# Performance work log

Hardware: AMD Instinct MI355X
Metric: run time of the kernel (lower is better)

## Reference

```python
import jax, jax.numpy as jnp
import numpy as np

HEADS = 4
HEAD_DIM = 32  # out_features // heads = 128 // 4


def setup_inputs() -> dict:
    key = jax.random.key(0)
    k1, k2, k3, k4 = jax.random.split(key, 4)
    N, IN_F = 200000, 128
    E = 500  # <= 1000 so no edge subsampling; loop covers min(E,500)=all edges
    x = jax.random.normal(k1, (N, IN_F), dtype=jnp.float32)
    edge_index = jax.random.randint(k2, (2, E), 0, N, dtype=jnp.int64)
    # Linear weight [out=heads*head_dim, in] as in torch nn.Linear
    W = jax.random.normal(k3, (HEADS * HEAD_DIM, IN_F), dtype=jnp.float32) * (1.0 / np.sqrt(IN_F))
    a = jax.random.normal(k4, (HEADS, 2 * HEAD_DIM), dtype=jnp.float32) * 0.1
    return {"x": x, "edge_index": edge_index, "W": W, "a": a}


def reference(x, edge_index, W, a):
    N = x.shape[0]
    h = (x @ W.T).reshape(N, HEADS, HEAD_DIM)  # [N, H, D]
    src, dst = edge_index[0], edge_index[1]
    h_src = h[src]  # [E, H, D]
    h_dst = h[dst]  # [E, H, D]
    edge_h = jnp.concatenate([h_src, h_dst], axis=-1)  # [E, H, 2D]
    attn = jnp.sum(edge_h * a, axis=-1)  # [E, H]
    attn = jax.nn.leaky_relu(attn, negative_slope=0.2)
    # out[dst] += 0.1 * attn * h[src], accumulated over duplicate dst
    out = h.at[dst].add(0.1 * attn[:, :, None] * h_src)
    return out.reshape(N, HEADS * HEAD_DIM)  # dropout is identity in eval
```

## Files before the change

kernel.cpp:

```cpp
#include <hip/hip_runtime.h>
#include <hip/hip_bf16.h>


typedef __attribute__((ext_vector_type(8))) short bf16x8;
typedef __attribute__((ext_vector_type(4))) float f32x4;

#define W_PAD 136

__global__ __launch_bounds__(256, 3) void gat_gemm_kernel(
    const float* __restrict__ x,
    const float* __restrict__ W,
    float* __restrict__ out,
    int N) {
  __shared__ __hip_bfloat16 Ws[128 * W_PAD];
  __shared__ __hip_bfloat16 Xs[64 * W_PAD];

  const int tid = threadIdx.x;

  #pragma unroll
  for (int it = 0; it < 16; ++it) {
    int seg = tid + it * 256;
    int row = seg >> 5;
    int off = (seg & 31) * 4;
    float4 v = *reinterpret_cast<const float4*>(&W[row * 128 + off]);
    union { ushort4 u4; __hip_bfloat16 h[4]; } wpk;
    wpk.h[0] = __float2bfloat16(v.x);
    wpk.h[1] = __float2bfloat16(v.y);
    wpk.h[2] = __float2bfloat16(v.z);
    wpk.h[3] = __float2bfloat16(v.w);
    *reinterpret_cast<ushort4*>(&Ws[row * W_PAD + off]) = wpk.u4;
  }
  __syncthreads();

  const int wave = tid >> 6;
  const int lane = tid & 63;
  const int m = lane & 15;
  const int q = lane >> 4;

  const int T64 = N >> 6;
  const int stride = (int)gridDim.x;
  int t = (int)blockIdx.x;

  float4 rA[8];
  {
    const float* xt = x + (long)t * 8192;
    #pragma unroll
    for (int i = 0; i < 8; ++i)
      rA[i] = *reinterpret_cast<const float4*>(xt + (i * 256 + tid) * 4);
  }

  while (true) {
    #pragma unroll
    for (int i = 0; i < 8; ++i) {
      int g = i * 256 + tid;
      union { ushort4 u4; __hip_bfloat16 h[4]; } p;
      p.h[0] = __float2bfloat16(rA[i].x);
      p.h[1] = __float2bfloat16(rA[i].y);
      p.h[2] = __float2bfloat16(rA[i].z);
      p.h[3] = __float2bfloat16(rA[i].w);
      *reinterpret_cast<ushort4*>(&Xs[(g >> 5) * W_PAD + (g & 31) * 4]) = p.u4;
    }

    const int tn = t + stride;
    if (tn < T64) {
      const float* xn = x + (long)tn * 8192;
      #pragma unroll
      for (int i = 0; i < 8; ++i)
        rA[i] = *reinterpret_cast<const float4*>(xn + (i * 256 + tid) * 4);
    }

    asm volatile("s_waitcnt lgkmcnt(0)" ::: "memory");
    __builtin_amdgcn_sched_barrier(0);
    __builtin_amdgcn_s_barrier();

    bf16x8 af[4];
    #pragma unroll
    for (int s = 0; s < 4; ++s)
      af[s] = *reinterpret_cast<const bf16x8*>(
          &Xs[(wave * 16 + m) * W_PAD + s * 32 + q * 8]);

    f32x4 acc[8];
    #pragma unroll
    for (int nt = 0; nt < 8; ++nt) acc[nt] = (f32x4){0.f, 0.f, 0.f, 0.f};
    #pragma unroll
    for (int s = 0; s < 4; ++s) {
      #pragma unroll
      for (int nt = 0; nt < 8; ++nt) {
        bf16x8 wfrag = *reinterpret_cast<const bf16x8*>(
            &Ws[(nt * 16 + m) * W_PAD + s * 32 + q * 8]);
        acc[nt] = __builtin_amdgcn_mfma_f32_16x16x32_bf16(wfrag, af[s],
                                                          acc[nt], 0, 0, 0);
      }
    }

    float* orow = out + (long)(t * 64 + wave * 16 + m) * 128 + q * 4;
    #pragma unroll
    for (int nt = 0; nt < 8; ++nt)
      *reinterpret_cast<f32x4*>(orow + nt * 16) = acc[nt];

    if (tn >= T64) break;

    __builtin_amdgcn_s_barrier();
    t = tn;
  }
}

__device__ __forceinline__ int detect_i64(const int* eidx) {
  int or_odd = 0;
  #pragma unroll
  for (int k = 0; k < 16; ++k) or_odd |= eidx[2 * k + 1];
  return or_odd == 0;
}

__global__ __launch_bounds__(128) void gat_edge_attn(
    const int* __restrict__ eidx,
    const float* __restrict__ a,
    const float* __restrict__ h,
    float* __restrict__ contrib,
    int E) {
  const int e = blockIdx.x;
  const int c = threadIdx.x;
  const bool is64 = detect_i64(eidx);
  const int src = is64 ? eidx[2 * e] : eidx[e];
  const int dst = is64 ? eidx[2 * (E + e)] : eidx[E + e];

  const float hs = h[(long)src * 128 + c];
  const float hd = h[(long)dst * 128 + c];

  const int head = c >> 5, d = c & 31;
  float term = a[head * 64 + d] * hs + a[head * 64 + 32 + d] * hd;
  term += __shfl_xor(term, 16);
  term += __shfl_xor(term, 8);
  term += __shfl_xor(term, 4);
  term += __shfl_xor(term, 2);
  term += __shfl_xor(term, 1);
  const float attn = term >= 0.f ? term : 0.2f * term;

  contrib[(long)e * 128 + c] = 0.1f * attn * hs;
}

__global__ __launch_bounds__(128) void gat_edge_scatter(
    const int* __restrict__ eidx,
    const float* __restrict__ contrib,
    float* __restrict__ out,
    int E) {
  const int e = blockIdx.x;
  const int c = threadIdx.x;
  const bool is64 = detect_i64(eidx);
  const int dst = is64 ? eidx[2 * (E + e)] : eidx[E + e];
  atomicAdd(&out[(long)dst * 128 + c], contrib[(long)e * 128 + c]);
}

extern "C" void kernel_launch(void* const* d_in, const int* in_sizes, int n_in,
                              void* d_out, int out_size, void* d_ws, size_t ws_size,
                              hipStream_t stream) {
  const float* x  = (const float*)d_in[0];
  const int* eidx = (const int*)d_in[1];
  const float* W  = (const float*)d_in[2];
  const float* a  = (const float*)d_in[3];
  float* out = (float*)d_out;
  float* contrib = (float*)d_ws;

  const int N = in_sizes[0] / 128;
  const int E = in_sizes[1] / 2;

  const int T64 = N / 64;
  int blocks = 768;
  if (blocks > T64) blocks = T64;
  gat_gemm_kernel<<<blocks, 256, 0, stream>>>(x, W, out, N);
  gat_edge_attn<<<E, 128, 0, stream>>>(eidx, a, out, contrib, E);
  gat_edge_scatter<<<E, 128, 0, stream>>>(eidx, contrib, out, E);
}
```

Measured before the change: 195.1 us.

## Give each wave its own 16-row tile to remove block barriers

```diff
diff --git a/kernel.cpp b/kernel.cpp
--- a/kernel.cpp
+++ b/kernel.cpp
@@ -13,7 +13,7 @@
     float* __restrict__ out,
     int N) {
   __shared__ __hip_bfloat16 Ws[128 * W_PAD];
-  __shared__ __hip_bfloat16 Xs[64 * W_PAD];
+  __shared__ __hip_bfloat16 Xs[4][16 * W_PAD];
 
   const int tid = threadIdx.x;
 
@@ -37,47 +37,49 @@
   const int m = lane & 15;
   const int q = lane >> 4;
 
-  const int T64 = N >> 6;
-  const int stride = (int)gridDim.x;
-  int t = (int)blockIdx.x;
+  __hip_bfloat16* xs = &Xs[wave][0];
 
-  float4 rA[8];
+  const int tiles = N >> 4;
+  const int gw = (int)gridDim.x * 4;
+  int t = (int)blockIdx.x * 4 + wave;
+  if (t >= tiles) return;
+
+  float4 raw[8];
   {
-    const float* xt = x + (long)t * 8192;
+    const float* xt = x + (long)t * 2048;
     #pragma unroll
     for (int i = 0; i < 8; ++i)
-      rA[i] = *reinterpret_cast<const float4*>(xt + (i * 256 + tid) * 4);
+      raw[i] = *reinterpret_cast<const float4*>(xt + (i * 64 + lane) * 4);
   }
 
   while (true) {
     #pragma unroll
     for (int i = 0; i < 8; ++i) {
-      int g = i * 256 + tid;
+      int g = i * 64 + lane;
       union { ushort4 u4; __hip_bfloat16 h[4]; } p;
-      p.h[0] = __float2bfloat16(rA[i].x);
-      p.h[1] = __float2bfloat16(rA[i].y);
-      p.h[2] = __float2bfloat16(rA[i].z);
-      p.h[3] = __float2bfloat16(rA[i].w);
-      *reinterpret_cast<ushort4*>(&Xs[(g >> 5) * W_PAD + (g & 31) * 4]) = p.u4;
+      p.h[0] = __float2bfloat16(raw[i].x);
+      p.h[1] = __float2bfloat16(raw[i].y);
+      p.h[2] = __float2bfloat16(raw[i].z);
+      p.h[3] = __float2bfloat16(raw[i].w);
+      *reinterpret_cast<ushort4*>(&xs[(g >> 5) * W_PAD + (g & 31) * 4]) = p.u4;
     }
 
-    const int tn = t + stride;
-    if (tn < T64) {
-      const float* xn = x + (long)tn * 8192;
+    const int tn = t + gw;
+    if (tn < tiles) {
+      const float* xt = x + (long)tn * 2048;
       #pragma unroll
       for (int i = 0; i < 8; ++i)
-        rA[i] = *reinterpret_cast<const float4*>(xn + (i * 256 + tid) * 4);
+        raw[i] = *reinterpret_cast<const float4*>(xt + (i * 64 + lane) * 4);
     }
 
     asm volatile("s_waitcnt lgkmcnt(0)" ::: "memory");
     __builtin_amdgcn_sched_barrier(0);
-    __builtin_amdgcn_s_barrier();
 
     bf16x8 af[4];
     #pragma unroll
     for (int s = 0; s < 4; ++s)
       af[s] = *reinterpret_cast<const bf16x8*>(
-          &Xs[(wave * 16 + m) * W_PAD + s * 32 + q * 8]);
+          &xs[m * W_PAD + s * 32 + q * 8]);
 
     f32x4 acc[8];
     #pragma unroll
@@ -93,14 +95,12 @@
       }
     }
 
-    float* orow = out + (long)(t * 64 + wave * 16 + m) * 128 + q * 4;
+    float* orow = out + (long)(t * 16 + m) * 128 + q * 4;
     #pragma unroll
     for (int nt = 0; nt < 8; ++nt)
       *reinterpret_cast<f32x4*>(orow + nt * 16) = acc[nt];
 
-    if (tn >= T64) break;
-
-    __builtin_amdgcn_s_barrier();
+    if (tn >= tiles) break;
     t = tn;
   }
 }
@@ -164,9 +164,9 @@
   const int N = in_sizes[0] / 128;
   const int E = in_sizes[1] / 2;
 
-  const int T64 = N / 64;
-  int blocks = 768;
-  if (blocks > T64) blocks = T64;
+  const int tiles = N / 16;
+  int blocks = (tiles + 3) / 4;
+  if (blocks > 768) blocks = 768;
   gat_gemm_kernel<<<blocks, 256, 0, stream>>>(x, W, out, N);
   gat_edge_attn<<<E, 128, 0, stream>>>(eidx, a, out, contrib, E);
   gat_edge_scatter<<<E, 128, 0, stream>>>(eidx, contrib, out, E);
```

Result: no change. 193.7 us (-0.7%).
